# Optimization experiments

Hardware: AMD Instinct MI355X
Metric: run time of the kernel (lower is better)

Reference implementation:

```python
import jax, jax.numpy as jnp
import numpy as np

LN_EPS = 1e-5  # torch nn.LayerNorm default
L2_EPS = 1e-12  # F.normalize default


def layer_norm(x, gamma, beta):
    mu = jnp.mean(x, axis=-1, keepdims=True)
    var = jnp.mean(jnp.square(x - mu), axis=-1, keepdims=True)
    return (x - mu) * jax.lax.rsqrt(var + LN_EPS) * gamma + beta


def l2_normalize(x):
    n = jnp.linalg.norm(x, axis=-1, keepdims=True)
    return x / jnp.maximum(n, L2_EPS)


def setup_inputs() -> dict:
    key = jax.random.key(0)
    k_x, k_mu = jax.random.split(key, 2)
    B, C, H, W = 4, 512, 128, 128
    K, M = 19, 5  # num_classes, num_components_per_class
    x = jax.random.normal(k_x, (B, C, H, W), dtype=jnp.float32)
    means = 0.02 * jax.random.normal(k_mu, (K, M, C), dtype=jnp.float32)  # trunc_normal_(std=0.02)
    diagonal = jnp.ones((K, M, C), dtype=jnp.float32)
    feat_gamma = jnp.ones((C,), dtype=jnp.float32)
    feat_beta = jnp.zeros((C,), dtype=jnp.float32)
    mask_gamma = jnp.ones((K,), dtype=jnp.float32)
    mask_beta = jnp.zeros((K,), dtype=jnp.float32)
    return dict(x=x, means=means, diagonal=diagonal,
                feat_gamma=feat_gamma, feat_beta=feat_beta,
                mask_gamma=mask_gamma, mask_beta=mask_beta)


def reference(x, means, diagonal, feat_gamma, feat_beta, mask_gamma, mask_beta):
    B, C, H, W = x.shape
    K, M, D = means.shape
    # rearrange 'b c h w -> (b h w) c'
    f = jnp.transpose(x, (0, 2, 3, 1)).reshape(-1, C)  # (N, D)
    f = layer_norm(f, feat_gamma, feat_beta)
    f = l2_normalize(f)
    # means are re-normalized in-place each forward
    mu = l2_normalize(means).reshape(K * M, D)          # (P, D), P = K*M
    sigma = diagonal.reshape(K * M, D)                  # diagonal scale (std)
    inv_var = 1.0 / jnp.square(sigma)
    # Mahalanobis distance via quadratic expansion (avoids (N,P,D) intermediate):
    # sum_d ((f - mu)/sigma)^2 = f^2 . iv - 2 f . (mu*iv) + sum(mu^2 * iv)
    q1 = jnp.square(f) @ inv_var.T                      # (N, P)
    q2 = f @ (mu * inv_var).T                           # (N, P)
    q3 = jnp.sum(jnp.square(mu) * inv_var, axis=-1)     # (P,)
    maha = q1 - 2.0 * q2 + q3[None, :]
    log_det = jnp.sum(jnp.log(sigma), axis=-1)          # sum log sigma, (P,)
    half_log2pi = 0.5 * D * jnp.log(2.0 * jnp.pi)
    log_prob = -0.5 * maha - log_det[None, :] - half_log2pi  # (N, P)
    log_prob = log_prob.reshape(-1, K, M)
    m_prob = jnp.max(log_prob, axis=-1)                 # amax over components, (N, K)
    out = layer_norm(m_prob, mask_gamma, mask_beta)
    # rearrange '(b h w) k -> b k h w'
    out_seg = jnp.transpose(out.reshape(B, H, W, K), (0, 3, 1, 2))
    return out_seg
```

## Files before the change

kernel.cpp:

```cpp
#include <hip/hip_runtime.h>
#include <math.h>

#define C_ 512
#define HW_ 16384
#define K_ 19
#define M_ 5
#define P_ 95
#define P2 96
#define TPX 32
#define NBLK 2048
#define HL2PI 470.49652900081467f

typedef __attribute__((ext_vector_type(8))) short short8;
typedef __attribute__((ext_vector_type(4))) float float4v;

static __device__ __forceinline__ short f2bf(float f) {
  unsigned u = __builtin_bit_cast(unsigned, f);
  unsigned r = (u + 0x7fffu + ((u >> 16) & 1u)) >> 16;
  return (short)r;
}

static __device__ __forceinline__ short8 sq8(short8 a) {
  short8 r;
#pragma unroll
  for (int j = 0; j < 8; j++) {
    float f = __builtin_bit_cast(float, ((unsigned)(unsigned short)a[j]) << 16);
    r[j] = f2bf(f * f);
  }
  return r;
}

__device__ __forceinline__ float block_reduce_sum(float v, volatile float* red) {
#pragma unroll
  for (int o = 32; o; o >>= 1) v += __shfl_down(v, o);
  const int lane = threadIdx.x & 63, wv = threadIdx.x >> 6;
  if (lane == 0) red[wv] = v;
  __syncthreads();
  float r = red[0] + red[1] + red[2] + red[3];
  __syncthreads();
  return r;
}

__global__ __launch_bounds__(256) void prep_kernel(
    const float* __restrict__ means, const float* __restrict__ diag,
    short* __restrict__ wbf, float* __restrict__ cterm) {
  const int p = blockIdx.x;
  const int tid = threadIdx.x;
  __shared__ float red[4];
  if (p >= P_) {
    for (int c = tid; c < C_; c += 256) {
      wbf[p * 1024 + c] = 0;
      wbf[p * 1024 + 512 + c] = 0;
    }
    if (tid == 0) cterm[p] = 0.f;
    return;
  }
  const float* mrow = means + (size_t)p * C_;
  const float* srow = diag + (size_t)p * C_;
  float m0 = mrow[tid], m1 = mrow[tid + 256];
  float ss = block_reduce_sum(m0 * m0 + m1 * m1, red);
  float rden = 1.f / fmaxf(sqrtf(ss), 1e-12f);
  float q3 = 0.f, ld = 0.f;
#pragma unroll
  for (int t = 0; t < 2; t++) {
    int c = tid + t * 256;
    float m = mrow[c], s = srow[c];
    float mu = m * rden;
    float iv = 1.f / (s * s);
    wbf[p * 1024 + c] = f2bf(iv);
    wbf[p * 1024 + 512 + c] = f2bf(mu * iv);
    q3 += mu * mu * iv;
    ld += logf(s);
  }
  q3 = block_reduce_sum(q3, red);
  ld = block_reduce_sum(ld, red);
  if (tid == 0) cterm[p] = -0.5f * q3 - ld - HL2PI;
}

__global__ __launch_bounds__(256) void main_kernel(
    const float* __restrict__ x,
    const float* __restrict__ fg, const float* __restrict__ fb,
    const float* __restrict__ mg, const float* __restrict__ mb,
    const short* __restrict__ wbf, const float* __restrict__ cterm,
    float* __restrict__ out) {
  __shared__ __align__(16) char raw[32768];
  __shared__ float red0[8 * TPX], red1[8 * TPX];
  __shared__ float meanA[TPX], rstdA[TPX], rnA[TPX], rn2A[TPX];
  __shared__ float mean2A[TPX], rstd2A[TPX];
  __shared__ float mpr[TPX * 20];

  const int tid = threadIdx.x;
  const int px = tid & 31, part = tid >> 5;
  const int wv = tid >> 6, lane = tid & 63;
  const int n0 = blockIdx.x * TPX;
  const int b = n0 >> 14;
  const int rem = n0 & 16383;
  const int h = rem >> 7;
  const int w0 = rem & 127;
  const int cbase = part * 64;
  const float* xp = x + (size_t)b * C_ * HW_ + h * 128 + w0 + px;

  {
    float s = 0.f, q = 0.f;
#pragma unroll 1
    for (int t16 = 0; t16 < 4; t16++) {
      float xv[16];
#pragma unroll
      for (int i = 0; i < 16; i++) xv[i] = xp[(size_t)(cbase + t16 * 16 + i) * HW_];
#pragma unroll
      for (int i = 0; i < 16; i++) {
        s += xv[i];
        q += xv[i] * xv[i];
      }
    }
    red0[part * 32 + px] = s;
    red1[part * 32 + px] = q;
  }
  __syncthreads();
  if (tid < 32) {
    float ss = 0.f, qq = 0.f;
#pragma unroll
    for (int i = 0; i < 8; i++) {
      ss += red0[i * 32 + tid];
      qq += red1[i * 32 + tid];
    }
    float mean = ss * (1.f / C_);
    float var = qq * (1.f / C_) - mean * mean;
    meanA[tid] = mean;
    rstdA[tid] = rsqrtf(var + 1e-5f);
  }
  __syncthreads();

  {
    const float mean = meanA[px], rstd = rstdA[px];
    float s2 = 0.f;
    const int t_ = px >> 4;
    const int lq = px & 15;
#pragma unroll 2
    for (int t8 = 0; t8 < 8; t8++) {
      const int c0 = cbase + t8 * 8;
      float xv[8];
#pragma unroll
      for (int j = 0; j < 8; j++) xv[j] = xp[(size_t)(c0 + j) * HW_];
      short8 vp;
#pragma unroll
      for (int j = 0; j < 8; j++) {
        float v = fmaf((xv[j] - mean) * rstd, fg[c0 + j], fb[c0 + j]);
        s2 += v * v;
        vp[j] = f2bf(v);
      }
      *(short8*)(raw + (((t_ * 16 + (c0 >> 5)) << 10) | (((c0 >> 3) & 3) << 8) | (lq << 4))) = vp;
    }
    red0[part * 32 + px] = s2;
  }
  __syncthreads();
  if (tid < 32) {
    float ss = 0.f;
#pragma unroll
    for (int i = 0; i < 8; i++) ss += red0[i * 32 + tid];
    float rn = 1.f / fmaxf(sqrtf(ss), 1e-12f);
    rnA[tid] = rn;
    rn2A[tid] = rn * rn;
  }
  __syncthreads();

  const int pbase = (wv & 1) * 3;
  const int khalf = wv >> 1;
  const int lm = lane & 15, lk = lane >> 4;
  float4v acc[3][2] = {{}, {}, {}};
  const short* wrow = wbf + (((pbase * 16 + lm) << 10) + (khalf << 9) + (lk << 3));
#pragma unroll 4
  for (int ksl = 0; ksl < 16; ksl++) {
    short8 a0 = *(const short8*)(wrow + ksl * 32);
    short8 a1 = *(const short8*)(wrow + 16384 + ksl * 32);
    short8 a2 = *(const short8*)(wrow + 32768 + ksl * 32);
    short8 b0 = *(const short8*)(raw + ((ksl << 10) | (lane << 4)));
    short8 b1 = *(const short8*)(raw + (((16 + ksl) << 10) | (lane << 4)));
    if (khalf == 0) {
      b0 = sq8(b0);
      b1 = sq8(b1);
    }
    acc[0][0] = __builtin_amdgcn_mfma_f32_16x16x32_bf16(a0, b0, acc[0][0], 0, 0, 0);
    acc[0][1] = __builtin_amdgcn_mfma_f32_16x16x32_bf16(a0, b1, acc[0][1], 0, 0, 0);
    acc[1][0] = __builtin_amdgcn_mfma_f32_16x16x32_bf16(a1, b0, acc[1][0], 0, 0, 0);
    acc[1][1] = __builtin_amdgcn_mfma_f32_16x16x32_bf16(a1, b1, acc[1][1], 0, 0, 0);
    acc[2][0] = __builtin_amdgcn_mfma_f32_16x16x32_bf16(a2, b0, acc[2][0], 0, 0, 0);
    acc[2][1] = __builtin_amdgcn_mfma_f32_16x16x32_bf16(a2, b1, acc[2][1], 0, 0, 0);
  }
  __syncthreads();
  float* lp = (float*)raw;

  if (khalf == 0) {
#pragma unroll
    for (int i = 0; i < 3; i++) {
      const int prow = (pbase + i) * 16 + lk * 4;
#pragma unroll
      for (int r = 0; r < 4; r++) {
        const float ct = cterm[prow + r];
#pragma unroll
        for (int t2 = 0; t2 < 2; t2++) {
          const int pxx = t2 * 16 + lm;
          lp[pxx * 100 + prow + r] = fmaf(-0.5f * rn2A[pxx], acc[i][t2][r], ct);
        }
      }
    }
  }
  __syncthreads();
  if (khalf == 1) {
#pragma unroll
    for (int i = 0; i < 3; i++) {
      const int prow = (pbase + i) * 16 + lk * 4;
#pragma unroll
      for (int r = 0; r < 4; r++) {
#pragma unroll
        for (int t2 = 0; t2 < 2; t2++) {
          const int pxx = t2 * 16 + lm;
          lp[pxx * 100 + prow + r] += rnA[pxx] * acc[i][t2][r];
        }
      }
    }
  }
  __syncthreads();

  for (int idx = tid; idx < TPX * K_; idx += 256) {
    const int pxx = idx / K_;
    const int k = idx - pxx * K_;
    const float* row = lp + pxx * 100 + k * M_;
    float mv = row[0];
#pragma unroll
    for (int m = 1; m < M_; m++) mv = fmaxf(mv, row[m]);
    mpr[pxx * 20 + k] = mv;
  }
  __syncthreads();
  if (tid < 32) {
    float ss = 0.f;
    for (int k = 0; k < K_; k++) ss += mpr[tid * 20 + k];
    float m2 = ss * (1.f / K_);
    float qq = 0.f;
    for (int k = 0; k < K_; k++) {
      float d = mpr[tid * 20 + k] - m2;
      qq += d * d;
    }
    mean2A[tid] = m2;
    rstd2A[tid] = rsqrtf(qq * (1.f / K_) + 1e-5f);
  }
  __syncthreads();
  float* obase = out + ((size_t)(b * K_) * 128 + h) * 128 + w0;
  for (int idx = tid; idx < TPX * K_; idx += 256) {
    const int k = idx >> 5, pxx = idx & 31;
    float v = fmaf((mpr[pxx * 20 + k] - mean2A[pxx]) * rstd2A[pxx], mg[k], mb[k]);
    obase[(size_t)k * HW_ + pxx] = v;
  }
}

extern "C" void kernel_launch(void* const* d_in, const int* in_sizes, int n_in,
                              void* d_out, int out_size, void* d_ws, size_t ws_size,
                              hipStream_t stream) {
  const float* x = (const float*)d_in[0];
  const float* means = (const float*)d_in[1];
  const float* diag = (const float*)d_in[2];
  const float* fg = (const float*)d_in[3];
  const float* fb = (const float*)d_in[4];
  const float* mg = (const float*)d_in[5];
  const float* mb = (const float*)d_in[6];
  float* out = (float*)d_out;

  short* wbf = (short*)d_ws;
  float* cterm = (float*)((char*)d_ws + (size_t)P2 * 1024 * 2);

  prep_kernel<<<P2, 256, 0, stream>>>(means, diag, wbf, cterm);
  main_kernel<<<NBLK, 256, 0, stream>>>(x, fg, fb, mg, mb, wbf, cterm, out);
}
```

Before: 81.63 us.

## Double pixels per block, keep x in registers, use packed bf16 conversion

Raises the tile to 64 pixels per block with 512 threads and 1024 blocks, and remaps waves so each wave covers one pixel pair, one component group and one k-half. Each thread now loads its 64 channels of x into registers once and reuses them for both LayerNorm passes, where before x was read from global memory twice. Float-to-bf16 conversion and squaring now use the hardware v_cvt_pk_bf16_f32 instruction instead of manual rounding. The costs are a 64KB LDS buffer and high register pressure from the 64-float array, which may lower occupancy or cause spills.

Result: faster. 76.21 us (-6.6%).

```diff
diff --git a/kernel.cpp b/kernel.cpp
--- a/kernel.cpp
+++ b/kernel.cpp
@@ -7,11 +7,12 @@
 #define M_ 5
 #define P_ 95
 #define P2 96
-#define TPX 32
-#define NBLK 2048
+#define TPX 64
+#define NBLK 1024
 #define HL2PI 470.49652900081467f
 
 typedef __attribute__((ext_vector_type(8))) short short8;
+typedef __attribute__((ext_vector_type(4))) int int4v;
 typedef __attribute__((ext_vector_type(4))) float float4v;
 
 static __device__ __forceinline__ short f2bf(float f) {
@@ -20,14 +21,23 @@
   return (short)r;
 }
 
+static __device__ __forceinline__ int pk2(float a, float b) {
+  int r;
+  asm("v_cvt_pk_bf16_f32 %0, %1, %2" : "=v"(r) : "v"(a), "v"(b));
+  return r;
+}
+
 static __device__ __forceinline__ short8 sq8(short8 a) {
-  short8 r;
-#pragma unroll
-  for (int j = 0; j < 8; j++) {
-    float f = __builtin_bit_cast(float, ((unsigned)(unsigned short)a[j]) << 16);
-    r[j] = f2bf(f * f);
-  }
-  return r;
+  int4v ai = __builtin_bit_cast(int4v, a);
+  int4v ri;
+#pragma unroll
+  for (int j = 0; j < 4; j++) {
+    unsigned u = (unsigned)ai[j];
+    float lo = __builtin_bit_cast(float, u << 16);
+    float hi = __builtin_bit_cast(float, u & 0xffff0000u);
+    ri[j] = pk2(lo * lo, hi * hi);
+  }
+  return __builtin_bit_cast(short8, ri);
 }
 
 __device__ __forceinline__ float block_reduce_sum(float v, volatile float* red) {
@@ -77,21 +87,22 @@
   if (tid == 0) cterm[p] = -0.5f * q3 - ld - HL2PI;
 }
 
-__global__ __launch_bounds__(256) void main_kernel(
+__global__ __launch_bounds__(512, 4) void main_kernel(
     const float* __restrict__ x,
     const float* __restrict__ fg, const float* __restrict__ fb,
     const float* __restrict__ mg, const float* __restrict__ mb,
     const short* __restrict__ wbf, const float* __restrict__ cterm,
     float* __restrict__ out) {
-  __shared__ __align__(16) char raw[32768];
+  __shared__ __align__(16) char raw[65536];
   __shared__ float red0[8 * TPX], red1[8 * TPX];
   __shared__ float meanA[TPX], rstdA[TPX], rnA[TPX], rn2A[TPX];
   __shared__ float mean2A[TPX], rstd2A[TPX];
   __shared__ float mpr[TPX * 20];
 
   const int tid = threadIdx.x;
-  const int px = tid & 31, part = tid >> 5;
-  const int wv = tid >> 6, lane = tid & 63;
+  const int px = tid & 63;
+  const int part = tid >> 6;
+  const int lane = tid & 63;
   const int n0 = blockIdx.x * TPX;
   const int b = n0 >> 14;
   const int rem = n0 & 16383;
@@ -100,29 +111,26 @@
   const int cbase = part * 64;
   const float* xp = x + (size_t)b * C_ * HW_ + h * 128 + w0 + px;
 
+  float xr[64];
+#pragma unroll
+  for (int i = 0; i < 64; i++) xr[i] = xp[(size_t)(cbase + i) * HW_];
   {
     float s = 0.f, q = 0.f;
-#pragma unroll 1
-    for (int t16 = 0; t16 < 4; t16++) {
-      float xv[16];
-#pragma unroll
-      for (int i = 0; i < 16; i++) xv[i] = xp[(size_t)(cbase + t16 * 16 + i) * HW_];
-#pragma unroll
-      for (int i = 0; i < 16; i++) {
-        s += xv[i];
-        q += xv[i] * xv[i];
-      }
-    }
-    red0[part * 32 + px] = s;
-    red1[part * 32 + px] = q;
-  }
-  __syncthreads();
-  if (tid < 32) {
+#pragma unroll
+    for (int i = 0; i < 64; i++) {
+      s += xr[i];
+      q += xr[i] * xr[i];
+    }
+    red0[part * 64 + px] = s;
+    red1[part * 64 + px] = q;
+  }
+  __syncthreads();
+  if (tid < 64) {
     float ss = 0.f, qq = 0.f;
 #pragma unroll
     for (int i = 0; i < 8; i++) {
-      ss += red0[i * 32 + tid];
-      qq += red1[i * 32 + tid];
+      ss += red0[i * 64 + tid];
+      qq += red1[i * 64 + tid];
     }
     float mean = ss * (1.f / C_);
     float var = qq * (1.f / C_) - mean * mean;
@@ -133,49 +141,52 @@
 
   {
     const float mean = meanA[px], rstd = rstdA[px];
+    const int t_ = px >> 4, lq = px & 15;
     float s2 = 0.f;
-    const int t_ = px >> 4;
-    const int lq = px & 15;
-#pragma unroll 2
+#pragma unroll
     for (int t8 = 0; t8 < 8; t8++) {
       const int c0 = cbase + t8 * 8;
-      float xv[8];
-#pragma unroll
-      for (int j = 0; j < 8; j++) xv[j] = xp[(size_t)(c0 + j) * HW_];
-      short8 vp;
+      float vv[8];
 #pragma unroll
       for (int j = 0; j < 8; j++) {
-        float v = fmaf((xv[j] - mean) * rstd, fg[c0 + j], fb[c0 + j]);
+        float v = fmaf((xr[t8 * 8 + j] - mean) * rstd, fg[c0 + j], fb[c0 + j]);
         s2 += v * v;
-        vp[j] = f2bf(v);
+        vv[j] = v;
       }
-      *(short8*)(raw + (((t_ * 16 + (c0 >> 5)) << 10) | (((c0 >> 3) & 3) << 8) | (lq << 4))) = vp;
-    }
-    red0[part * 32 + px] = s2;
-  }
-  __syncthreads();
-  if (tid < 32) {
+      int4v pk;
+#pragma unroll
+      for (int j2 = 0; j2 < 4; j2++) pk[j2] = pk2(vv[2 * j2], vv[2 * j2 + 1]);
+      *(int4v*)(raw + (((t_ * 16 + (c0 >> 5)) << 10) | (((c0 >> 3) & 3) << 8) | (lq << 4))) = pk;
+    }
+    red0[part * 64 + px] = s2;
+  }
+  __syncthreads();
+  if (tid < 64) {
     float ss = 0.f;
 #pragma unroll
-    for (int i = 0; i < 8; i++) ss += red0[i * 32 + tid];
+    for (int i = 0; i < 8; i++) ss += red0[i * 64 + tid];
     float rn = 1.f / fmaxf(sqrtf(ss), 1e-12f);
     rnA[tid] = rn;
     rn2A[tid] = rn * rn;
   }
   __syncthreads();
 
-  const int pbase = (wv & 1) * 3;
-  const int khalf = wv >> 1;
+  const int wv = part;
+  const int khalf = wv >> 2;
+  const int pbase = ((wv >> 1) & 1) * 3;
+  const int pxpair = wv & 1;
   const int lm = lane & 15, lk = lane >> 4;
   float4v acc[3][2] = {{}, {}, {}};
   const short* wrow = wbf + (((pbase * 16 + lm) << 10) + (khalf << 9) + (lk << 3));
+  const int base0 = (pxpair * 2) * 16384;
+  const int base1 = (pxpair * 2 + 1) * 16384;
 #pragma unroll 4
   for (int ksl = 0; ksl < 16; ksl++) {
     short8 a0 = *(const short8*)(wrow + ksl * 32);
     short8 a1 = *(const short8*)(wrow + 16384 + ksl * 32);
     short8 a2 = *(const short8*)(wrow + 32768 + ksl * 32);
-    short8 b0 = *(const short8*)(raw + ((ksl << 10) | (lane << 4)));
-    short8 b1 = *(const short8*)(raw + (((16 + ksl) << 10) | (lane << 4)));
+    short8 b0 = *(const short8*)(raw + base0 + (ksl << 10) + (lane << 4));
+    short8 b1 = *(const short8*)(raw + base1 + (ksl << 10) + (lane << 4));
     if (khalf == 0) {
       b0 = sq8(b0);
       b1 = sq8(b1);
@@ -199,7 +210,7 @@
         const float ct = cterm[prow + r];
 #pragma unroll
         for (int t2 = 0; t2 < 2; t2++) {
-          const int pxx = t2 * 16 + lm;
+          const int pxx = (pxpair * 2 + t2) * 16 + lm;
           lp[pxx * 100 + prow + r] = fmaf(-0.5f * rn2A[pxx], acc[i][t2][r], ct);
         }
       }
@@ -214,7 +225,7 @@
       for (int r = 0; r < 4; r++) {
 #pragma unroll
         for (int t2 = 0; t2 < 2; t2++) {
-          const int pxx = t2 * 16 + lm;
+          const int pxx = (pxpair * 2 + t2) * 16 + lm;
           lp[pxx * 100 + prow + r] += rnA[pxx] * acc[i][t2][r];
         }
       }
@@ -222,7 +233,7 @@
   }
   __syncthreads();
 
-  for (int idx = tid; idx < TPX * K_; idx += 256) {
+  for (int idx = tid; idx < TPX * K_; idx += 512) {
     const int pxx = idx / K_;
     const int k = idx - pxx * K_;
     const float* row = lp + pxx * 100 + k * M_;
@@ -232,7 +243,7 @@
     mpr[pxx * 20 + k] = mv;
   }
   __syncthreads();
-  if (tid < 32) {
+  if (tid < 64) {
     float ss = 0.f;
     for (int k = 0; k < K_; k++) ss += mpr[tid * 20 + k];
     float m2 = ss * (1.f / K_);
@@ -246,8 +257,8 @@
   }
   __syncthreads();
   float* obase = out + ((size_t)(b * K_) * 128 + h) * 128 + w0;
-  for (int idx = tid; idx < TPX * K_; idx += 256) {
-    const int k = idx >> 5, pxx = idx & 31;
+  for (int idx = tid; idx < TPX * K_; idx += 512) {
+    const int k = idx >> 6, pxx = idx & 63;
     float v = fmaf((mpr[pxx * 20 + k] - mean2A[pxx]) * rstd2A[pxx], mg[k], mb[k]);
     obase[(size_t)k * HW_ + pxx] = v;
   }
@@ -269,5 +280,5 @@
   float* cterm = (float*)((char*)d_ws + (size_t)P2 * 1024 * 2);
 
   prep_kernel<<<P2, 256, 0, stream>>>(means, diag, wbf, cterm);
-  main_kernel<<<NBLK, 256, 0, stream>>>(x, fg, fb, mg, mb, wbf, cterm, out);
-}
+  main_kernel<<<NBLK, 512, 0, stream>>>(x, fg, fb, mg, mb, wbf, cterm, out);
+}
```

## Halve LDS footprint by staging normalized features in two K-halves interleaved with MFMA

Applied to the files above, without the earlier changes.

The bf16 feature tile is now built and consumed in two 256-channel halves, each staged into a 16KB LDS buffer followed by the MFMA loop for that half. This halves shared memory and reuses it for the reduction and max-prob scratch, so more blocks can be resident per CU. The L2-norm reduction moves after the GEMM. Packing to bf16 now uses the hardware v_cvt_pk_bf16_f32 instruction instead of manual rounding. The cost is extra barriers per half and a second pass over x that is no longer fully decoupled from the matrix math.

After: 81.10 us. No clear change (-0.7%).

```diff
diff --git a/kernel.cpp b/kernel.cpp
--- a/kernel.cpp
+++ b/kernel.cpp
@@ -12,6 +12,7 @@
 #define HL2PI 470.49652900081467f
 
 typedef __attribute__((ext_vector_type(8))) short short8;
+typedef __attribute__((ext_vector_type(4))) int int4v;
 typedef __attribute__((ext_vector_type(4))) float float4v;
 
 static __device__ __forceinline__ short f2bf(float f) {
@@ -20,14 +21,23 @@
   return (short)r;
 }
 
+static __device__ __forceinline__ int pk2(float a, float b) {
+  int r;
+  asm("v_cvt_pk_bf16_f32 %0, %1, %2" : "=v"(r) : "v"(a), "v"(b));
+  return r;
+}
+
 static __device__ __forceinline__ short8 sq8(short8 a) {
-  short8 r;
-#pragma unroll
-  for (int j = 0; j < 8; j++) {
-    float f = __builtin_bit_cast(float, ((unsigned)(unsigned short)a[j]) << 16);
-    r[j] = f2bf(f * f);
-  }
-  return r;
+  int4v ai = __builtin_bit_cast(int4v, a);
+  int4v ri;
+#pragma unroll
+  for (int j = 0; j < 4; j++) {
+    unsigned u = (unsigned)ai[j];
+    float lo = __builtin_bit_cast(float, u << 16);
+    float hi = __builtin_bit_cast(float, u & 0xffff0000u);
+    ri[j] = pk2(lo * lo, hi * hi);
+  }
+  return __builtin_bit_cast(short8, ri);
 }
 
 __device__ __forceinline__ float block_reduce_sum(float v, volatile float* red) {
@@ -83,11 +93,10 @@
     const float* __restrict__ mg, const float* __restrict__ mb,
     const short* __restrict__ wbf, const float* __restrict__ cterm,
     float* __restrict__ out) {
-  __shared__ __align__(16) char raw[32768];
-  __shared__ float red0[8 * TPX], red1[8 * TPX];
+  __shared__ __align__(16) char raw[16384];
+  __shared__ float red1[256];
   __shared__ float meanA[TPX], rstdA[TPX], rnA[TPX], rn2A[TPX];
   __shared__ float mean2A[TPX], rstd2A[TPX];
-  __shared__ float mpr[TPX * 20];
 
   const int tid = threadIdx.x;
   const int px = tid & 31, part = tid >> 5;
@@ -97,24 +106,25 @@
   const int rem = n0 & 16383;
   const int h = rem >> 7;
   const int w0 = rem & 127;
-  const int cbase = part * 64;
+  const int t_ = px >> 4, lq = px & 15;
   const float* xp = x + (size_t)b * C_ * HW_ + h * 128 + w0 + px;
 
+  float* red0 = (float*)raw;
   {
     float s = 0.f, q = 0.f;
 #pragma unroll 1
-    for (int t16 = 0; t16 < 4; t16++) {
-      float xv[16];
-#pragma unroll
-      for (int i = 0; i < 16; i++) xv[i] = xp[(size_t)(cbase + t16 * 16 + i) * HW_];
-#pragma unroll
-      for (int i = 0; i < 16; i++) {
-        s += xv[i];
-        q += xv[i] * xv[i];
-      }
-    }
-    red0[part * 32 + px] = s;
-    red1[part * 32 + px] = q;
+    for (int g = 0; g < 8; g++) {
+      float xv[8];
+#pragma unroll
+      for (int j = 0; j < 8; j++) xv[j] = xp[(size_t)(part * 64 + g * 8 + j) * HW_];
+#pragma unroll
+      for (int j = 0; j < 8; j++) {
+        s += xv[j];
+        q = fmaf(xv[j], xv[j], q);
+      }
+    }
+    red0[tid] = s;
+    red1[tid] = q;
   }
   __syncthreads();
   if (tid < 32) {
@@ -128,39 +138,6 @@
     float var = qq * (1.f / C_) - mean * mean;
     meanA[tid] = mean;
     rstdA[tid] = rsqrtf(var + 1e-5f);
-  }
-  __syncthreads();
-
-  {
-    const float mean = meanA[px], rstd = rstdA[px];
-    float s2 = 0.f;
-    const int t_ = px >> 4;
-    const int lq = px & 15;
-#pragma unroll 2
-    for (int t8 = 0; t8 < 8; t8++) {
-      const int c0 = cbase + t8 * 8;
-      float xv[8];
-#pragma unroll
-      for (int j = 0; j < 8; j++) xv[j] = xp[(size_t)(c0 + j) * HW_];
-      short8 vp;
-#pragma unroll
-      for (int j = 0; j < 8; j++) {
-        float v = fmaf((xv[j] - mean) * rstd, fg[c0 + j], fb[c0 + j]);
-        s2 += v * v;
-        vp[j] = f2bf(v);
-      }
-      *(short8*)(raw + (((t_ * 16 + (c0 >> 5)) << 10) | (((c0 >> 3) & 3) << 8) | (lq << 4))) = vp;
-    }
-    red0[part * 32 + px] = s2;
-  }
-  __syncthreads();
-  if (tid < 32) {
-    float ss = 0.f;
-#pragma unroll
-    for (int i = 0; i < 8; i++) ss += red0[i * 32 + tid];
-    float rn = 1.f / fmaxf(sqrtf(ss), 1e-12f);
-    rnA[tid] = rn;
-    rn2A[tid] = rn * rn;
   }
   __syncthreads();
 
@@ -169,26 +146,68 @@
   const int lm = lane & 15, lk = lane >> 4;
   float4v acc[3][2] = {{}, {}, {}};
   const short* wrow = wbf + (((pbase * 16 + lm) << 10) + (khalf << 9) + (lk << 3));
+  float s2 = 0.f;
+  const float mean = meanA[px], rstd = rstdA[px];
+
+#pragma unroll 1
+  for (int half = 0; half < 2; half++) {
+#pragma unroll
+    for (int j8 = 0; j8 < 4; j8++) {
+      const int c0 = half * 256 + part * 32 + j8 * 8;
+      float xv[8];
+#pragma unroll
+      for (int j = 0; j < 8; j++) xv[j] = xp[(size_t)(c0 + j) * HW_];
+      float vv[8];
+#pragma unroll
+      for (int j = 0; j < 8; j++) {
+        float v = fmaf((xv[j] - mean) * rstd, fg[c0 + j], fb[c0 + j]);
+        s2 = fmaf(v, v, s2);
+        vv[j] = v;
+      }
+      int4v pk;
+#pragma unroll
+      for (int j2 = 0; j2 < 4; j2++) pk[j2] = pk2(vv[2 * j2], vv[2 * j2 + 1]);
+      const int ksl = (c0 >> 5) & 7;
+      *(int4v*)(raw + (((t_ * 8 + ksl) << 10) | (((c0 >> 3) & 3) << 8) | (lq << 4))) = pk;
+    }
+    __syncthreads();
+
 #pragma unroll 4
-  for (int ksl = 0; ksl < 16; ksl++) {
-    short8 a0 = *(const short8*)(wrow + ksl * 32);
-    short8 a1 = *(const short8*)(wrow + 16384 + ksl * 32);
-    short8 a2 = *(const short8*)(wrow + 32768 + ksl * 32);
-    short8 b0 = *(const short8*)(raw + ((ksl << 10) | (lane << 4)));
-    short8 b1 = *(const short8*)(raw + (((16 + ksl) << 10) | (lane << 4)));
-    if (khalf == 0) {
-      b0 = sq8(b0);
-      b1 = sq8(b1);
-    }
-    acc[0][0] = __builtin_amdgcn_mfma_f32_16x16x32_bf16(a0, b0, acc[0][0], 0, 0, 0);
-    acc[0][1] = __builtin_amdgcn_mfma_f32_16x16x32_bf16(a0, b1, acc[0][1], 0, 0, 0);
-    acc[1][0] = __builtin_amdgcn_mfma_f32_16x16x32_bf16(a1, b0, acc[1][0], 0, 0, 0);
-    acc[1][1] = __builtin_amdgcn_mfma_f32_16x16x32_bf16(a1, b1, acc[1][1], 0, 0, 0);
-    acc[2][0] = __builtin_amdgcn_mfma_f32_16x16x32_bf16(a2, b0, acc[2][0], 0, 0, 0);
-    acc[2][1] = __builtin_amdgcn_mfma_f32_16x16x32_bf16(a2, b1, acc[2][1], 0, 0, 0);
-  }
-  __syncthreads();
+    for (int ksl = 0; ksl < 8; ksl++) {
+      const int kk = half * 8 + ksl;
+      short8 a0 = *(const short8*)(wrow + kk * 32);
+      short8 a1 = *(const short8*)(wrow + 16384 + kk * 32);
+      short8 a2 = *(const short8*)(wrow + 32768 + kk * 32);
+      short8 b0 = *(const short8*)(raw + ((ksl << 10) | (lane << 4)));
+      short8 b1 = *(const short8*)(raw + (((8 + ksl) << 10) | (lane << 4)));
+      if (khalf == 0) {
+        b0 = sq8(b0);
+        b1 = sq8(b1);
+      }
+      acc[0][0] = __builtin_amdgcn_mfma_f32_16x16x32_bf16(a0, b0, acc[0][0], 0, 0, 0);
+      acc[0][1] = __builtin_amdgcn_mfma_f32_16x16x32_bf16(a0, b1, acc[0][1], 0, 0, 0);
+      acc[1][0] = __builtin_amdgcn_mfma_f32_16x16x32_bf16(a1, b0, acc[1][0], 0, 0, 0);
+      acc[1][1] = __builtin_amdgcn_mfma_f32_16x16x32_bf16(a1, b1, acc[1][1], 0, 0, 0);
+      acc[2][0] = __builtin_amdgcn_mfma_f32_16x16x32_bf16(a2, b0, acc[2][0], 0, 0, 0);
+      acc[2][1] = __builtin_amdgcn_mfma_f32_16x16x32_bf16(a2, b1, acc[2][1], 0, 0, 0);
+    }
+    __syncthreads();
+  }
+
+  red1[tid] = s2;
+  __syncthreads();
+  if (tid < 32) {
+    float ss = 0.f;
+#pragma unroll
+    for (int i = 0; i < 8; i++) ss += red1[i * 32 + tid];
+    float rn = 1.f / fmaxf(sqrtf(ss), 1e-12f);
+    rnA[tid] = rn;
+    rn2A[tid] = rn * rn;
+  }
+  __syncthreads();
+
   float* lp = (float*)raw;
+  float* mpr = (float*)(raw + 12800);
 
   if (khalf == 0) {
 #pragma unroll
```
